# Optimization experiments

Hardware: AMD Instinct MI355X
Metric: run time of the kernel (lower is better)

The kernel has to match this reference:

```python
import jax, jax.numpy as jnp
import numpy as np

B, S, E, H = 8, 3072, 512, 8  # batch, total seq (3 chunks of 1024), emb_size, num_heads


def setup_inputs() -> dict:
    key = jax.random.key(0)
    ks = jax.random.split(key, 9)
    sc = 0.02  # weight init scale
    return {
        "x": jax.random.normal(ks[0], (B, S, E), jnp.float32),
        "Wq": jax.random.normal(ks[1], (3, E, E), jnp.float32) * sc,
        "bq": jax.random.normal(ks[2], (3, E), jnp.float32) * sc,
        "Wk": jax.random.normal(ks[3], (3, E, E), jnp.float32) * sc,
        "bk": jax.random.normal(ks[4], (3, E), jnp.float32) * sc,
        "Wv": jax.random.normal(ks[5], (3, E, E), jnp.float32) * sc,
        "bv": jax.random.normal(ks[6], (3, E), jnp.float32) * sc,
        "Wp": jax.random.normal(ks[7], (3, E, E), jnp.float32) * sc,
        "bp": jax.random.normal(ks[8], (3, E), jnp.float32) * sc,
    }


def reference(x, Wq, bq, Wk, bk, Wv, bv, Wp, bp):
    b, s, e = x.shape
    d = e // H
    # split into 3 chunks along seq: xc[c] is chunk c, shape [b, n, e]
    xc = jnp.stack(jnp.split(x, 3, axis=1))  # [3, b, n, e]

    def lin(W, bias):  # torch Linear: x @ W.T + b, per chunk
        return jnp.einsum('cbne,cfe->cbnf', xc, W) + bias[:, None, None, :]

    def heads(t):  # [3, b, n, e] -> [3, b, h, n, d]
        c, bb, n, _ = t.shape
        return t.reshape(c, bb, n, H, d).transpose(0, 1, 3, 2, 4)

    q = heads(lin(Wq, bq))
    k = heads(lin(Wk, bk))
    v = heads(lin(Wv, bv))

    # rotated cross-chunk pairing (faithful to source):
    # out1 = attn(q2, k3, v3); out2 = attn(q3, k1, v1); out3 = attn(q1, k2, v2)
    q_sel = q[jnp.array([1, 2, 0])]
    k_sel = k[jnp.array([2, 0, 1])]
    v_sel = v[jnp.array([2, 0, 1])]

    scaling = jnp.sqrt(jnp.float32(e))  # note: sqrt(emb_size), not sqrt(head_dim)
    energy = jnp.einsum('cbhqd,cbhkd->cbhqk', q_sel, k_sel) / scaling
    att = jax.nn.softmax(energy, axis=-1)  # dropout: eval-mode identity
    out = jnp.einsum('cbhqk,cbhkd->cbhqd', att, v_sel)
    out = out.transpose(0, 1, 3, 2, 4).reshape(3, b, s // 3, e)  # merge heads
    out = jnp.einsum('cbne,cfe->cbnf', out, Wp) + bp[:, None, None, :]
    return jnp.concatenate([out[0], out[1], out[2]], axis=1)  # [b, s, e]
```

## Files before the change

kernel.cpp:

```cpp
#include <hip/hip_runtime.h>
#include <hip/hip_bf16.h>


typedef __attribute__((ext_vector_type(8))) short short8v;
typedef __attribute__((ext_vector_type(4))) float float4v;
typedef __attribute__((ext_vector_type(4))) unsigned short ushort4v;
typedef __attribute__((ext_vector_type(4))) unsigned int uint4v;

#define CHUNKS 3
#define BATCH 8
#define SEQ 3072
#define EMB 512
#define NH 8
#define HD 64
#define NCK 1024
#define MTOT (BATCH*SEQ)
#define QKV_ELEMS (CHUNKS*BATCH*NH*NCK*HD)
#define WELEMS (CHUNKS*EMB*EMB)
#define QSCALE 0.06375872465f

__device__ __forceinline__ unsigned short f2b(float f) {
  union { float f; unsigned int i; } x; x.f = f;
  unsigned int r = x.i + 0x7FFFu + ((x.i >> 16) & 1u);
  return (unsigned short)(r >> 16);
}
__device__ __forceinline__ unsigned int pack2r(float a, float b) {
  union { float f; unsigned int u; } xa, xb; xa.f = a; xb.f = b;
  return __builtin_amdgcn_perm(xb.u + 0x8000u, xa.u + 0x8000u, 0x07060302u);
}
__device__ __forceinline__ void gld_lds16(const unsigned short* g, unsigned short* l) {
  __builtin_amdgcn_global_load_lds(
      (const __attribute__((address_space(1))) unsigned int*)g,
      (__attribute__((address_space(3))) unsigned int*)l, 16, 0, 0);
}
#define MFMA(a, b, c) __builtin_amdgcn_mfma_f32_16x16x32_bf16(a, b, c, 0, 0, 0)

__global__ __launch_bounds__(256) void conv_x(
    const float* __restrict__ src, unsigned short* __restrict__ dst)
{
  size_t i = ((size_t)blockIdx.x * 256 + threadIdx.x) * 8;
  float4 a = *(const float4*)&src[i];
  float4 b = *(const float4*)&src[i + 4];
  uint4v p;
  p[0] = pack2r(a.x, a.y); p[1] = pack2r(a.z, a.w);
  p[2] = pack2r(b.x, b.y); p[3] = pack2r(b.z, b.w);
  *(uint4v*)&dst[i] = p;
}

__global__ __launch_bounds__(256) void conv_w(
    const float* __restrict__ s0, const float* __restrict__ s1,
    const float* __restrict__ s2, const float* __restrict__ s3,
    unsigned short* __restrict__ dst)
{
  const int z = blockIdx.y;
  const float* s = (z == 0) ? s0 : (z == 1) ? s1 : (z == 2) ? s2 : s3;
  size_t i = ((size_t)blockIdx.x * 256 + threadIdx.x) * 8;
  float4 a = *(const float4*)&s[i];
  float4 b = *(const float4*)&s[i + 4];
  uint4v p;
  p[0] = pack2r(a.x, a.y); p[1] = pack2r(a.z, a.w);
  p[2] = pack2r(b.x, b.y); p[3] = pack2r(b.z, b.w);
  *(uint4v*)&dst[(size_t)z * WELEMS + i] = p;
}

__global__ __launch_bounds__(256) void qkv_gemm(
    const unsigned short* __restrict__ xb, const unsigned short* __restrict__ Wb,
    const float* __restrict__ bq, const float* __restrict__ bk,
    const float* __restrict__ bv,
    unsigned short* __restrict__ qt, unsigned short* __restrict__ kt,
    unsigned short* __restrict__ vt)
{
  const int tid = threadIdx.x;
  const int w = tid >> 6, l = tid & 63;
  const int ln = l & 15, qu = l >> 4;
  const int sr = l >> 3, kbl = l & 7;
  const int row0 = blockIdx.x * 128;
  const int col0 = blockIdx.y * 128;
  const int z = blockIdx.z;
  const int bglob = row0 / SEQ;
  const int c = (row0 % SEQ) / NCK;
  const int n0 = row0 % NCK;
  const unsigned short* W = Wb + (size_t)z * WELEMS + c * EMB * EMB;
  const float* bias = (z == 0 ? bq : (z == 1 ? bk : bv)) + c * EMB;
  const float oscale = (z == 0) ? QSCALE : 1.0f;

  __shared__ unsigned short As[128 * 64];
  __shared__ unsigned short Bs[128 * 64];

  const int xo = (w & 1) * 64, fo = (w >> 1) * 64;

  float4v acc[4][4];
#pragma unroll
  for (int i = 0; i < 4; ++i)
#pragma unroll
    for (int j = 0; j < 4; ++j) acc[i][j] = (float4v){0.f, 0.f, 0.f, 0.f};

  for (int k0 = 0; k0 < EMB; k0 += 64) {
    __syncthreads();
#pragma unroll
    for (int s = 0; s < 4; ++s) {
      int rbase = w * 32 + s * 8;
      int r = rbase + sr;
      int kb_g = kbl ^ sr;
      gld_lds16(&xb[(size_t)(row0 + r) * EMB + k0 + kb_g * 8], &As[rbase * 64]);
      gld_lds16(&W [(size_t)(col0 + r) * EMB + k0 + kb_g * 8], &Bs[rbase * 64]);
    }
    __syncthreads();
#pragma unroll
    for (int ks = 0; ks < 2; ++ks) {
      short8v xf[4], wf[4];
#pragma unroll
      for (int i = 0; i < 4; ++i) {
        int rx = xo + 16 * i + ln;
        xf[i] = *(const short8v*)&As[rx * 64 + (((ks * 4 + qu) ^ (rx & 7)) * 8)];
        int rw = fo + 16 * i + ln;
        wf[i] = *(const short8v*)&Bs[rw * 64 + (((ks * 4 + qu) ^ (rw & 7)) * 8)];
      }
      if (z <= 1) {
#pragma unroll
        for (int i = 0; i < 4; ++i)
#pragma unroll
          for (int j = 0; j < 4; ++j) acc[i][j] = MFMA(wf[j], xf[i], acc[i][j]);
      } else {
#pragma unroll
        for (int i = 0; i < 4; ++i)
#pragma unroll
          for (int j = 0; j < 4; ++j) acc[i][j] = MFMA(xf[i], wf[j], acc[i][j]);
      }
    }
  }

  if (z <= 1) {
    unsigned short* outp = (z == 0) ? qt : kt;
#pragma unroll
    for (int j = 0; j < 4; ++j) {
      int f0 = col0 + fo + 16 * j + 4 * qu;
      float4 b4 = *(const float4*)&bias[f0];
      int hh = f0 >> 6, dd0 = f0 & 63;
      size_t base = ((size_t)((c * 8 + bglob) * 8 + hh)) << 16;
#pragma unroll
      for (int i = 0; i < 4; ++i) {
        int n = n0 + xo + 16 * i + ln;
        ushort4v p;
#pragma unroll
        for (int r = 0; r < 4; ++r)
          p[r] = f2b((acc[i][j][r] + ((const float*)&b4)[r]) * oscale);
        *(ushort4v*)&outp[base + (size_t)n * 64 + dd0] = p;
      }
    }
  } else {
#pragma unroll
    for (int i = 0; i < 4; ++i) {
      int nn0 = n0 + xo + 16 * i + 4 * qu;
#pragma unroll
      for (int j = 0; j < 4; ++j) {
        int f = col0 + fo + 16 * j + ln;
        int hh = f >> 6, dd = f & 63;
        float bvv = bias[f];
        size_t base = ((size_t)((c * 8 + bglob) * 8 + hh)) << 16;
        ushort4v p;
#pragma unroll
        for (int r = 0; r < 4; ++r) p[r] = f2b(acc[i][j][r] + bvv);
        *(ushort4v*)&vt[base + (size_t)dd * 1024 + nn0] = p;
      }
    }
  }
}

__global__ __launch_bounds__(512) void attn_kernel(
    const unsigned short* __restrict__ qt,
    const unsigned short* __restrict__ kt,
    const unsigned short* __restrict__ vt,
    unsigned short* __restrict__ attnb)
{
  const int tid = threadIdx.x;
  const int w = tid >> 6, l = tid & 63;
  const int ln = l & 15, qu = l >> 4;
  const int sr = l >> 3, kbl = l & 7;
  const int bid = blockIdx.x;
  const int hd = bid % 192;
  const int q0 = (bid / 192) * 256;
  const int co = hd >> 6;
  const int b  = (hd >> 3) & 7;
  const int h  = hd & 7;
  const int cq = (co + 1) % 3, ckv = (co + 2) % 3;
  const unsigned short* Qg = qt + ((size_t)((cq  * 8 + b) * 8 + h) << 16);
  const unsigned short* Kg = kt + ((size_t)((ckv * 8 + b) * 8 + h) << 16);
  const unsigned short* Vg = vt + ((size_t)((ckv * 8 + b) * 8 + h) << 16);

  __shared__ unsigned short Ks[64 * 64];
  __shared__ unsigned short Vs[64 * 64];

  short8v qf[2][2];
#pragma unroll
  for (int nt = 0; nt < 2; ++nt)
#pragma unroll
    for (int ks = 0; ks < 2; ++ks)
      qf[nt][ks] = *(const short8v*)&Qg[(size_t)(q0 + w * 32 + nt * 16 + ln) * 64 + ks * 32 + qu * 8];

  short8v onesf;
#pragma unroll
  for (int i = 0; i < 8; ++i) onesf[i] = (short)0x3F80;

  float4v acc_o[4][2];
#pragma unroll
  for (int i = 0; i < 4; ++i)
#pragma unroll
    for (int j = 0; j < 2; ++j) acc_o[i][j] = (float4v){0.f, 0.f, 0.f, 0.f};
  float4v acc_l[2];
  acc_l[0] = (float4v){0.f, 0.f, 0.f, 0.f};
  acc_l[1] = (float4v){0.f, 0.f, 0.f, 0.f};

  for (int kt0 = 0; kt0 < NCK; kt0 += 64) {
    __syncthreads();
    {
      int r = w * 8;
      gld_lds16(&Kg[(size_t)(kt0 + r + sr) * 64 + ((kbl ^ sr) * 8)], &Ks[r * 64]);
      gld_lds16(&Vg[(size_t)(r + sr) * 1024 + kt0 + ((kbl ^ sr) * 8)], &Vs[r * 64]);
    }
    __syncthreads();

    float4v sacc[4][2];
#pragma unroll
    for (int mt = 0; mt < 4; ++mt)
#pragma unroll
      for (int nt = 0; nt < 2; ++nt) sacc[mt][nt] = (float4v){0.f, 0.f, 0.f, 0.f};
    __builtin_amdgcn_s_setprio(1);
#pragma unroll
    for (int ks = 0; ks < 2; ++ks) {
#pragma unroll
      for (int mt = 0; mt < 4; ++mt) {
        int key = 16 * mt + ln;
        short8v kf = *(const short8v*)&Ks[key * 64 + (((ks * 4 + qu) ^ (key & 7)) * 8)];
#pragma unroll
        for (int nt = 0; nt < 2; ++nt)
          sacc[mt][nt] = MFMA(kf, qf[nt][ks], sacc[mt][nt]);
      }
    }
    __builtin_amdgcn_s_setprio(0);

#pragma unroll
    for (int ks2 = 0; ks2 < 2; ++ks2) {
      short8v pf[2];
#pragma unroll
      for (int nt = 0; nt < 2; ++nt) {
        float4v s0v = sacc[2 * ks2][nt];
        float4v s1v = sacc[2 * ks2 + 1][nt];
        float a0 = __builtin_amdgcn_exp2f(s0v[0]);
        float a1 = __builtin_amdgcn_exp2f(s0v[1]);
        float a2 = __builtin_amdgcn_exp2f(s0v[2]);
        float a3 = __builtin_amdgcn_exp2f(s0v[3]);
        float b0 = __builtin_amdgcn_exp2f(s1v[0]);
        float b1 = __builtin_amdgcn_exp2f(s1v[1]);
        float b2 = __builtin_amdgcn_exp2f(s1v[2]);
        float b3 = __builtin_amdgcn_exp2f(s1v[3]);
        unsigned int m00 = pack2r(a0, a1);
        unsigned int m01 = pack2r(a2, a3);
        unsigned int m10 = pack2r(b0, b1);
        unsigned int m11 = pack2r(b2, b3);
        asm("v_permlane32_swap_b32 %0, %1" : "+v"(m00), "+v"(m10));
        asm("v_permlane32_swap_b32 %0, %1" : "+v"(m01), "+v"(m11));
        asm("v_permlane16_swap_b32 %0, %1" : "+v"(m00), "+v"(m10));
        asm("v_permlane16_swap_b32 %0, %1" : "+v"(m01), "+v"(m11));
        uint4v t; t[0] = m00; t[1] = m01; t[2] = m10; t[3] = m11;
        pf[nt] = __builtin_bit_cast(short8v, t);
      }
      __builtin_amdgcn_s_setprio(1);
#pragma unroll
      for (int nt = 0; nt < 2; ++nt)
        acc_l[nt] = MFMA(onesf, pf[nt], acc_l[nt]);
#pragma unroll
      for (int mt2 = 0; mt2 < 4; ++mt2) {
        int dd = 16 * mt2 + ln;
        short8v vf = *(const short8v*)&Vs[dd * 64 + (((ks2 * 4 + qu) ^ (dd & 7)) * 8)];
#pragma unroll
        for (int nt = 0; nt < 2; ++nt)
          acc_o[mt2][nt] = MFMA(vf, pf[nt], acc_o[mt2][nt]);
      }
      __builtin_amdgcn_s_setprio(0);
    }
  }

  float inv[2];
  inv[0] = 1.0f / acc_l[0][0];
  inv[1] = 1.0f / acc_l[1][0];
  unsigned short* Og = attnb + (size_t)((co * 8 + b)) * NCK * EMB + h * HD;
#pragma unroll
  for (int mt = 0; mt < 4; ++mt) {
    int dd0 = 16 * mt + 4 * qu;
#pragma unroll
    for (int nt = 0; nt < 2; ++nt) {
      int q_glob = q0 + w * 32 + nt * 16 + ln;
      ushort4v p;
#pragma unroll
      for (int r = 0; r < 4; ++r) p[r] = f2b(acc_o[mt][nt][r] * inv[nt]);
      *(ushort4v*)&Og[(size_t)q_glob * EMB + dd0] = p;
    }
  }
}

__global__ __launch_bounds__(256) void proj_gemm(
    const unsigned short* __restrict__ attnb,
    const unsigned short* __restrict__ Wpb, const float* __restrict__ bp,
    float* __restrict__ out)
{
  const int tid = threadIdx.x;
  const int w = tid >> 6, l = tid & 63;
  const int ln = l & 15, qu = l >> 4;
  const int sr = l >> 3, kbl = l & 7;
  const int row0 = blockIdx.x * 128;
  const int col0 = blockIdx.y * 128;
  const int c = row0 >> 13;
  const int bglob = (row0 >> 10) & 7;
  const int n0 = row0 & 1023;
  const unsigned short* W = Wpb + c * EMB * EMB;
  const float* bias = bp + c * EMB;

  __shared__ unsigned short As[128 * 64];
  __shared__ unsigned short Bs[128 * 64];

  const int xo = (w & 1) * 64, fo = (w >> 1) * 64;

  float4v acc[4][4];
#pragma unroll
  for (int i = 0; i < 4; ++i)
#pragma unroll
    for (int j = 0; j < 4; ++j) acc[i][j] = (float4v){0.f, 0.f, 0.f, 0.f};

  for (int k0 = 0; k0 < EMB; k0 += 64) {
    __syncthreads();
#pragma unroll
    for (int s = 0; s < 4; ++s) {
      int rbase = w * 32 + s * 8;
      int r = rbase + sr;
      int kb_g = kbl ^ sr;
      gld_lds16(&attnb[(size_t)(row0 + r) * EMB + k0 + kb_g * 8], &As[rbase * 64]);
      gld_lds16(&W    [(size_t)(col0 + r) * EMB + k0 + kb_g * 8], &Bs[rbase * 64]);
    }
    __syncthreads();
#pragma unroll
    for (int ks = 0; ks < 2; ++ks) {
      short8v xf[4], wf[4];
#pragma unroll
      for (int i = 0; i < 4; ++i) {
        int rx = xo + 16 * i + ln;
        xf[i] = *(const short8v*)&As[rx * 64 + (((ks * 4 + qu) ^ (rx & 7)) * 8)];
        int rw = fo + 16 * i + ln;
        wf[i] = *(const short8v*)&Bs[rw * 64 + (((ks * 4 + qu) ^ (rw & 7)) * 8)];
      }
#pragma unroll
      for (int i = 0; i < 4; ++i)
#pragma unroll
        for (int j = 0; j < 4; ++j) acc[i][j] = MFMA(wf[j], xf[i], acc[i][j]);
    }
  }

#pragma unroll
  for (int j = 0; j < 4; ++j) {
    int f0 = col0 + fo + 16 * j + 4 * qu;
    float4 b4 = *(const float4*)&bias[f0];
#pragma unroll
    for (int i = 0; i < 4; ++i) {
      int srow = bglob * SEQ + c * NCK + n0 + xo + 16 * i + ln;
      float4 o;
      o.x = acc[i][j][0] + b4.x;
      o.y = acc[i][j][1] + b4.y;
      o.z = acc[i][j][2] + b4.z;
      o.w = acc[i][j][3] + b4.w;
      *(float4*)&out[(size_t)srow * EMB + f0] = o;
    }
  }
}

extern "C" void kernel_launch(void* const* d_in, const int* in_sizes, int n_in,
                              void* d_out, int out_size, void* d_ws, size_t ws_size,
                              hipStream_t stream) {
  (void)in_sizes; (void)n_in; (void)out_size; (void)ws_size;
  const float* x  = (const float*)d_in[0];
  const float* Wq = (const float*)d_in[1];
  const float* bq = (const float*)d_in[2];
  const float* Wk = (const float*)d_in[3];
  const float* bk = (const float*)d_in[4];
  const float* Wv = (const float*)d_in[5];
  const float* bv = (const float*)d_in[6];
  const float* Wp = (const float*)d_in[7];
  const float* bp = (const float*)d_in[8];
  float* out = (float*)d_out;

  unsigned short* Wb   = (unsigned short*)d_ws;
  unsigned short* qt   = Wb + 4 * (size_t)WELEMS;
  unsigned short* kt   = qt + QKV_ELEMS;
  unsigned short* vt   = kt + QKV_ELEMS;
  unsigned short* attn = vt + QKV_ELEMS;
  unsigned short* xbf  = attn;

  conv_x<<<QKV_ELEMS / (256 * 8), 256, 0, stream>>>(x, xbf);
  conv_w<<<dim3(WELEMS / (256 * 8), 4), 256, 0, stream>>>(Wq, Wk, Wv, Wp, Wb);
  qkv_gemm<<<dim3(MTOT / 128, EMB / 128, 3), 256, 0, stream>>>(
      xbf, Wb, bq, bk, bv, qt, kt, vt);
  attn_kernel<<<(NCK / 256) * CHUNKS * BATCH * NH, 512, 0, stream>>>(qt, kt, vt, attn);
  proj_gemm<<<dim3(MTOT / 128, EMB / 128), 256, 0, stream>>>(attn, Wb + 3 * (size_t)WELEMS, bp, out);
}
```

Measured before the change: 277.1 us.

## Double-buffer LDS tiles in QKV, attention and projection kernels

Each of the three main loops now uses two LDS buffers: it issues global-to-LDS loads for the next tile before computing on the current one, and uses a single barrier per iteration instead of two. The aim is to hide global memory latency behind MFMA work. This doubles LDS use per block, which may reduce occupancy. Visibility of the async LDS writes relies on the barrier at the end of each iteration.

```diff
diff --git a/kernel.cpp b/kernel.cpp
--- a/kernel.cpp
+++ b/kernel.cpp
@@ -62,6 +62,19 @@
   p[2] = pack2r(b.x, b.y); p[3] = pack2r(b.z, b.w);
   *(uint4v*)&dst[(size_t)z * WELEMS + i] = p;
 }
+
+#define QKV_STAGE(buf, k0v) do {                                               \
+  _Pragma("unroll")                                                            \
+  for (int s = 0; s < 4; ++s) {                                                \
+    int rbase = w * 32 + s * 8;                                                \
+    int r = rbase + sr;                                                        \
+    int kb_g = kbl ^ sr;                                                       \
+    gld_lds16(&Ag[(size_t)(row0 + r) * EMB + (k0v) + kb_g * 8],                \
+              &As[buf][rbase * 64]);                                           \
+    gld_lds16(&W [(size_t)(col0 + r) * EMB + (k0v) + kb_g * 8],                \
+              &Bs[buf][rbase * 64]);                                           \
+  }                                                                            \
+} while (0)
 
 __global__ __launch_bounds__(256) void qkv_gemm(
     const unsigned short* __restrict__ xb, const unsigned short* __restrict__ Wb,
@@ -80,12 +93,13 @@
   const int bglob = row0 / SEQ;
   const int c = (row0 % SEQ) / NCK;
   const int n0 = row0 % NCK;
+  const unsigned short* Ag = xb;
   const unsigned short* W = Wb + (size_t)z * WELEMS + c * EMB * EMB;
   const float* bias = (z == 0 ? bq : (z == 1 ? bk : bv)) + c * EMB;
   const float oscale = (z == 0) ? QSCALE : 1.0f;
 
-  __shared__ unsigned short As[128 * 64];
-  __shared__ unsigned short Bs[128 * 64];
+  __shared__ unsigned short As[2][128 * 64];
+  __shared__ unsigned short Bs[2][128 * 64];
 
   const int xo = (w & 1) * 64, fo = (w >> 1) * 64;
 
@@ -95,26 +109,20 @@
 #pragma unroll
     for (int j = 0; j < 4; ++j) acc[i][j] = (float4v){0.f, 0.f, 0.f, 0.f};
 
+  QKV_STAGE(0, 0);
+  __syncthreads();
+  int cur = 0;
   for (int k0 = 0; k0 < EMB; k0 += 64) {
-    __syncthreads();
-#pragma unroll
-    for (int s = 0; s < 4; ++s) {
-      int rbase = w * 32 + s * 8;
-      int r = rbase + sr;
-      int kb_g = kbl ^ sr;
-      gld_lds16(&xb[(size_t)(row0 + r) * EMB + k0 + kb_g * 8], &As[rbase * 64]);
-      gld_lds16(&W [(size_t)(col0 + r) * EMB + k0 + kb_g * 8], &Bs[rbase * 64]);
-    }
-    __syncthreads();
+    if (k0 + 64 < EMB) QKV_STAGE(cur ^ 1, k0 + 64);
 #pragma unroll
     for (int ks = 0; ks < 2; ++ks) {
       short8v xf[4], wf[4];
 #pragma unroll
       for (int i = 0; i < 4; ++i) {
         int rx = xo + 16 * i + ln;
-        xf[i] = *(const short8v*)&As[rx * 64 + (((ks * 4 + qu) ^ (rx & 7)) * 8)];
+        xf[i] = *(const short8v*)&As[cur][rx * 64 + (((ks * 4 + qu) ^ (rx & 7)) * 8)];
         int rw = fo + 16 * i + ln;
-        wf[i] = *(const short8v*)&Bs[rw * 64 + (((ks * 4 + qu) ^ (rw & 7)) * 8)];
+        wf[i] = *(const short8v*)&Bs[cur][rw * 64 + (((ks * 4 + qu) ^ (rw & 7)) * 8)];
       }
       if (z <= 1) {
 #pragma unroll
@@ -128,6 +136,8 @@
           for (int j = 0; j < 4; ++j) acc[i][j] = MFMA(xf[i], wf[j], acc[i][j]);
       }
     }
+    __syncthreads();
+    cur ^= 1;
   }
 
   if (z <= 1) {
@@ -166,6 +176,14 @@
     }
   }
 }
+
+#define ATTN_STAGE(buf, kt0v) do {                                             \
+  int r = w * 8;                                                               \
+  gld_lds16(&Kg[(size_t)((kt0v) + r + sr) * 64 + ((kbl ^ sr) * 8)],            \
+            &Ks[buf][r * 64]);                                                 \
+  gld_lds16(&Vg[(size_t)(r + sr) * 1024 + (kt0v) + ((kbl ^ sr) * 8)],          \
+            &Vs[buf][r * 64]);                                                 \
+} while (0)
 
 __global__ __launch_bounds__(512) void attn_kernel(
     const unsigned short* __restrict__ qt,
@@ -188,8 +206,8 @@
   const unsigned short* Kg = kt + ((size_t)((ckv * 8 + b) * 8 + h) << 16);
   const unsigned short* Vg = vt + ((size_t)((ckv * 8 + b) * 8 + h) << 16);
 
-  __shared__ unsigned short Ks[64 * 64];
-  __shared__ unsigned short Vs[64 * 64];
+  __shared__ unsigned short Ks[2][64 * 64];
+  __shared__ unsigned short Vs[2][64 * 64];
 
   short8v qf[2][2];
 #pragma unroll
@@ -211,14 +229,11 @@
   acc_l[0] = (float4v){0.f, 0.f, 0.f, 0.f};
   acc_l[1] = (float4v){0.f, 0.f, 0.f, 0.f};
 
+  ATTN_STAGE(0, 0);
+  __syncthreads();
+  int cur = 0;
   for (int kt0 = 0; kt0 < NCK; kt0 += 64) {
-    __syncthreads();
-    {
-      int r = w * 8;
-      gld_lds16(&Kg[(size_t)(kt0 + r + sr) * 64 + ((kbl ^ sr) * 8)], &Ks[r * 64]);
-      gld_lds16(&Vg[(size_t)(r + sr) * 1024 + kt0 + ((kbl ^ sr) * 8)], &Vs[r * 64]);
-    }
-    __syncthreads();
+    if (kt0 + 64 < NCK) ATTN_STAGE(cur ^ 1, kt0 + 64);
 
     float4v sacc[4][2];
 #pragma unroll
@@ -231,7 +246,7 @@
 #pragma unroll
       for (int mt = 0; mt < 4; ++mt) {
         int key = 16 * mt + ln;
-        short8v kf = *(const short8v*)&Ks[key * 64 + (((ks * 4 + qu) ^ (key & 7)) * 8)];
+        short8v kf = *(const short8v*)&Ks[cur][key * 64 + (((ks * 4 + qu) ^ (key & 7)) * 8)];
 #pragma unroll
         for (int nt = 0; nt < 2; ++nt)
           sacc[mt][nt] = MFMA(kf, qf[nt][ks], sacc[mt][nt]);
@@ -272,13 +287,16 @@
 #pragma unroll
       for (int mt2 = 0; mt2 < 4; ++mt2) {
         int dd = 16 * mt2 + ln;
-        short8v vf = *(const short8v*)&Vs[dd * 64 + (((ks2 * 4 + qu) ^ (dd & 7)) * 8)];
+        short8v vf = *(const short8v*)&Vs[cur][dd * 64 + (((ks2 * 4 + qu) ^ (dd & 7)) * 8)];
 #pragma unroll
         for (int nt = 0; nt < 2; ++nt)
           acc_o[mt2][nt] = MFMA(vf, pf[nt], acc_o[mt2][nt]);
       }
       __builtin_amdgcn_s_setprio(0);
     }
+
+    __syncthreads();
+    cur ^= 1;
   }
 
   float inv[2];
@@ -313,11 +331,12 @@
   const int c = row0 >> 13;
   const int bglob = (row0 >> 10) & 7;
   const int n0 = row0 & 1023;
+  const unsigned short* Ag = attnb;
   const unsigned short* W = Wpb + c * EMB * EMB;
   const float* bias = bp + c * EMB;
 
-  __shared__ unsigned short As[128 * 64];
-  __shared__ unsigned short Bs[128 * 64];
+  __shared__ unsigned short As[2][128 * 64];
+  __shared__ unsigned short Bs[2][128 * 64];
 
   const int xo = (w & 1) * 64, fo = (w >> 1) * 64;
 
@@ -327,32 +346,28 @@
 #pragma unroll
     for (int j = 0; j < 4; ++j) acc[i][j] = (float4v){0.f, 0.f, 0.f, 0.f};
 
+  QKV_STAGE(0, 0);
+  __syncthreads();
+  int cur = 0;
   for (int k0 = 0; k0 < EMB; k0 += 64) {
-    __syncthreads();
-#pragma unroll
-    for (int s = 0; s < 4; ++s) {
-      int rbase = w * 32 + s * 8;
-      int r = rbase + sr;
-      int kb_g = kbl ^ sr;
-      gld_lds16(&attnb[(size_t)(row0 + r) * EMB + k0 + kb_g * 8], &As[rbase * 64]);
-      gld_lds16(&W    [(size_t)(col0 + r) * EMB + k0 + kb_g * 8], &Bs[rbase * 64]);
-    }
-    __syncthreads();
+    if (k0 + 64 < EMB) QKV_STAGE(cur ^ 1, k0 + 64);
 #pragma unroll
     for (int ks = 0; ks < 2; ++ks) {
       short8v xf[4], wf[4];
 #pragma unroll
       for (int i = 0; i < 4; ++i) {
         int rx = xo + 16 * i + ln;
-        xf[i] = *(const short8v*)&As[rx * 64 + (((ks * 4 + qu) ^ (rx & 7)) * 8)];
+        xf[i] = *(const short8v*)&As[cur][rx * 64 + (((ks * 4 + qu) ^ (rx & 7)) * 8)];
         int rw = fo + 16 * i + ln;
-        wf[i] = *(const short8v*)&Bs[rw * 64 + (((ks * 4 + qu) ^ (rw & 7)) * 8)];
+        wf[i] = *(const short8v*)&Bs[cur][rw * 64 + (((ks * 4 + qu) ^ (rw & 7)) * 8)];
       }
 #pragma unroll
       for (int i = 0; i < 4; ++i)
 #pragma unroll
         for (int j = 0; j < 4; ++j) acc[i][j] = MFMA(wf[j], xf[i], acc[i][j]);
     }
+    __syncthreads();
+    cur ^= 1;
   }
 
 #pragma unroll
```

Result: slower. 303.3 us (+9.4%).

## Double-buffer K/V tiles in attention and remap GEMM blocks for XCD locality

Applied to the files above, without the earlier changes.

The attention kernel now keeps two LDS buffers for the K/V tiles and prefetches the next tile while computing on the current one, which cuts the per-iteration barriers from two to one. The goal is to hide global-to-LDS load latency behind the MFMA work. Both GEMM kernels switch to a 1-D grid with a permuted block index, so blocks dispatched round-robin across the 8 XCDs get contiguous tiles and share A rows in L2. The cost is doubled LDS use in attention, which may lower occupancy.

```diff
diff --git a/kernel.cpp b/kernel.cpp
--- a/kernel.cpp
+++ b/kernel.cpp
@@ -74,9 +74,11 @@
   const int w = tid >> 6, l = tid & 63;
   const int ln = l & 15, qu = l >> 4;
   const int sr = l >> 3, kbl = l & 7;
-  const int row0 = blockIdx.x * 128;
-  const int col0 = blockIdx.y * 128;
-  const int z = blockIdx.z;
+  const int bid = blockIdx.x;
+  const int lin = (bid & 7) * 288 + (bid >> 3);
+  const int col0 = (lin & 3) * 128;
+  const int z = (lin >> 2) % 3;
+  const int row0 = (lin / 12) * 128;
   const int bglob = row0 / SEQ;
   const int c = (row0 % SEQ) / NCK;
   const int n0 = row0 % NCK;
@@ -166,6 +168,14 @@
     }
   }
 }
+
+#define ATTN_STAGE(buf, kt0v) do {                                             \
+  int r = w * 8;                                                               \
+  gld_lds16(&Kg[(size_t)((kt0v) + r + sr) * 64 + ((kbl ^ sr) * 8)],            \
+            &Ks[buf][r * 64]);                                                 \
+  gld_lds16(&Vg[(size_t)(r + sr) * 1024 + (kt0v) + ((kbl ^ sr) * 8)],          \
+            &Vs[buf][r * 64]);                                                 \
+} while (0)
 
 __global__ __launch_bounds__(512) void attn_kernel(
     const unsigned short* __restrict__ qt,
@@ -188,8 +198,8 @@
   const unsigned short* Kg = kt + ((size_t)((ckv * 8 + b) * 8 + h) << 16);
   const unsigned short* Vg = vt + ((size_t)((ckv * 8 + b) * 8 + h) << 16);
 
-  __shared__ unsigned short Ks[64 * 64];
-  __shared__ unsigned short Vs[64 * 64];
+  __shared__ unsigned short Ks[2][64 * 64];
+  __shared__ unsigned short Vs[2][64 * 64];
 
   short8v qf[2][2];
 #pragma unroll
@@ -211,14 +221,11 @@
   acc_l[0] = (float4v){0.f, 0.f, 0.f, 0.f};
   acc_l[1] = (float4v){0.f, 0.f, 0.f, 0.f};
 
+  ATTN_STAGE(0, 0);
+  __syncthreads();
+  int cur = 0;
   for (int kt0 = 0; kt0 < NCK; kt0 += 64) {
-    __syncthreads();
-    {
-      int r = w * 8;
-      gld_lds16(&Kg[(size_t)(kt0 + r + sr) * 64 + ((kbl ^ sr) * 8)], &Ks[r * 64]);
-      gld_lds16(&Vg[(size_t)(r + sr) * 1024 + kt0 + ((kbl ^ sr) * 8)], &Vs[r * 64]);
-    }
-    __syncthreads();
+    if (kt0 + 64 < NCK) ATTN_STAGE(cur ^ 1, kt0 + 64);
 
     float4v sacc[4][2];
 #pragma unroll
@@ -231,7 +238,7 @@
 #pragma unroll
       for (int mt = 0; mt < 4; ++mt) {
         int key = 16 * mt + ln;
-        short8v kf = *(const short8v*)&Ks[key * 64 + (((ks * 4 + qu) ^ (key & 7)) * 8)];
+        short8v kf = *(const short8v*)&Ks[cur][key * 64 + (((ks * 4 + qu) ^ (key & 7)) * 8)];
 #pragma unroll
         for (int nt = 0; nt < 2; ++nt)
           sacc[mt][nt] = MFMA(kf, qf[nt][ks], sacc[mt][nt]);
@@ -272,13 +279,16 @@
 #pragma unroll
       for (int mt2 = 0; mt2 < 4; ++mt2) {
         int dd = 16 * mt2 + ln;
-        short8v vf = *(const short8v*)&Vs[dd * 64 + (((ks2 * 4 + qu) ^ (dd & 7)) * 8)];
+        short8v vf = *(const short8v*)&Vs[cur][dd * 64 + (((ks2 * 4 + qu) ^ (dd & 7)) * 8)];
 #pragma unroll
         for (int nt = 0; nt < 2; ++nt)
           acc_o[mt2][nt] = MFMA(vf, pf[nt], acc_o[mt2][nt]);
       }
       __builtin_amdgcn_s_setprio(0);
     }
+
+    __syncthreads();
+    cur ^= 1;
   }
 
   float inv[2];
@@ -308,8 +318,10 @@
   const int w = tid >> 6, l = tid & 63;
   const int ln = l & 15, qu = l >> 4;
   const int sr = l >> 3, kbl = l & 7;
-  const int row0 = blockIdx.x * 128;
-  const int col0 = blockIdx.y * 128;
+  const int bid = blockIdx.x;
+  const int lin = (bid & 7) * 96 + (bid >> 3);
+  const int col0 = (lin & 3) * 128;
+  const int row0 = (lin >> 2) * 128;
   const int c = row0 >> 13;
   const int bglob = (row0 >> 10) & 7;
   const int n0 = row0 & 1023;
@@ -396,8 +408,8 @@
 
   conv_x<<<QKV_ELEMS / (256 * 8), 256, 0, stream>>>(x, xbf);
   conv_w<<<dim3(WELEMS / (256 * 8), 4), 256, 0, stream>>>(Wq, Wk, Wv, Wp, Wb);
-  qkv_gemm<<<dim3(MTOT / 128, EMB / 128, 3), 256, 0, stream>>>(
+  qkv_gemm<<<(MTOT / 128) * (EMB / 128) * 3, 256, 0, stream>>>(
       xbf, Wb, bq, bk, bv, qt, kt, vt);
   attn_kernel<<<(NCK / 256) * CHUNKS * BATCH * NH, 512, 0, stream>>>(qt, kt, vt, attn);
-  proj_gemm<<<dim3(MTOT / 128, EMB / 128), 256, 0, stream>>>(attn, Wb + 3 * (size_t)WELEMS, bp, out);
-}
+  proj_gemm<<<(MTOT / 128) * (EMB / 128), 256, 0, stream>>>(attn, Wb + 3 * (size_t)WELEMS, bp, out);
+}
```

After: 267.1 us. 1.04x faster.
